# Optimization experiments

Hardware: AMD Instinct MI355X
Metric: run time of the kernel (lower is better)

## Reference

```python
import jax, jax.numpy as jnp
import numpy as np

N_RETRIEVAL = 10  # config['n_retrieval']


def setup_inputs() -> dict:
    key = jax.random.key(0)
    kq, kk, ko = jax.random.split(key, 3)
    Q, N, D = 256, 10000, 128
    C, H, W = 4, 84, 84
    q = jax.random.normal(kq, (Q, D), dtype=jnp.float32)
    k = jax.random.normal(kk, (N, D), dtype=jnp.float32)
    obs = jax.random.uniform(ko, (N, C, H, W), dtype=jnp.float32)
    return {"q": q, "k": k, "obs": obs}


def reference(q, k, obs):
    # Squared euclidean distances [Q, N] (same ordering as sklearn's
    # euclidean kneighbors; sqrt is monotone so top-k indices match).
    q2 = jnp.sum(q * q, axis=1, keepdims=True)            # [Q, 1]
    k2 = jnp.sum(k * k, axis=1)                            # [N]
    sqdist = q2 - 2.0 * (q @ k.T) + k2[None, :]            # [Q, N]
    # n_retrieval smallest distances -> indices [Q, K]
    _, indices = jax.lax.top_k(-sqdist, N_RETRIEVAL)
    # Gather observations: [Q, K, C, H, W]
    selected_obs = obs[indices]
    # permute(1, 0, 2, 3, 4) -> [K, Q, C, H, W]
    selected_obs = jnp.transpose(selected_obs, (1, 0, 2, 3, 4))
    return selected_obs
```

## Files before the change

### kernel.cpp

```cpp
#include <hip/hip_runtime.h>
#include <stdint.h>

#define QCNT 256
#define NKEYS 10000
#define DDIM 128
#define KSEL 10
#define OBSROW 28224

typedef float f4v __attribute__((ext_vector_type(4)));
typedef float f32x4 __attribute__((ext_vector_type(4)));
typedef _Float16 f16x8 __attribute__((ext_vector_type(8)));

#define QTILE 16
#define KCHUNK 48
#define NTILES 3
#define NCHUNK_M ((NKEYS + KCHUNK - 1) / KCHUNK)
#define LISTM 10

__device__ inline unsigned long long enc_key(float d, int n) {
  unsigned u = __float_as_uint(d);
  u ^= (unsigned)((int)u >> 31) | 0x80000000u;
  return ((unsigned long long)u << 32) | (unsigned)n;
}

__device__ inline unsigned long long wave_min_u64(unsigned long long w) {
#pragma unroll
  for (int off = 1; off < 64; off <<= 1) {
    unsigned long long o =
        (unsigned long long)__shfl_xor((long long)w, off, 64);
    if (o < w) w = o;
  }
  return w;
}

__device__ inline void insert10(unsigned long long best[LISTM],
                                unsigned long long key) {
  if (key < best[LISTM - 1]) {
    best[LISTM - 1] = key;
#pragma unroll
    for (int s = LISTM - 1; s >= 1; --s) {
      if (best[s] < best[s - 1]) {
        unsigned long long t = best[s];
        best[s] = best[s - 1];
        best[s - 1] = t;
      }
    }
  }
}

__global__ __launch_bounds__(64) void knn_part_fused(
    const float* __restrict__ q, const float* __restrict__ k,
    unsigned long long* __restrict__ part) {
  const int qt   = blockIdx.x;
  const int ch   = blockIdx.y;
  const int lane = threadIdx.x;
  const int lq   = lane & 15;
  const int lk8  = (lane >> 4) * 8;
  const int q0   = qt * QTILE;

  f16x8 bh[4], bl[4];
  {
    const float* qrow = q + (size_t)(q0 + lq) * DDIM + lk8;
#pragma unroll
    for (int kc = 0; kc < 4; ++kc) {
      f4v v0 = *(const f4v*)(qrow + kc * 32);
      f4v v1 = *(const f4v*)(qrow + kc * 32 + 4);
      float e[8] = {v0.x, v0.y, v0.z, v0.w, v1.x, v1.y, v1.z, v1.w};
#pragma unroll
      for (int j = 0; j < 8; ++j) {
        _Float16 h = (_Float16)e[j];
        bh[kc][j]  = h;
        bl[kc][j]  = (_Float16)(e[j] - (float)h);
      }
    }
  }

  unsigned long long list[LISTM];
#pragma unroll
  for (int s = 0; s < LISTM; ++s) list[s] = ~0ULL;

  const int kbase = ch * KCHUNK;
#pragma unroll
  for (int t = 0; t < NTILES; ++t) {
    const int tb  = kbase + t * 16;
    int row       = tb + lq;
    if (row > NKEYS - 1) row = NKEYS - 1;
    const float* arow = k + (size_t)row * DDIM + lk8;

    f32x4 acc = {0.f, 0.f, 0.f, 0.f};
    float k2p = 0.f;
#pragma unroll
    for (int kc = 0; kc < 4; ++kc) {
      f4v a0 = *(const f4v*)(arow + kc * 32);
      f4v a1 = *(const f4v*)(arow + kc * 32 + 4);
      float e[8] = {a0.x, a0.y, a0.z, a0.w, a1.x, a1.y, a1.z, a1.w};
      f16x8 ah, al;
#pragma unroll
      for (int j = 0; j < 8; ++j) {
        _Float16 h = (_Float16)e[j];
        ah[j]      = h;
        al[j]      = (_Float16)(e[j] - (float)h);
        k2p        = fmaf(e[j], e[j], k2p);
      }
      acc = __builtin_amdgcn_mfma_f32_16x16x32_f16(ah, bh[kc], acc, 0, 0, 0);
      acc = __builtin_amdgcn_mfma_f32_16x16x32_f16(ah, bl[kc], acc, 0, 0, 0);
      acc = __builtin_amdgcn_mfma_f32_16x16x32_f16(al, bh[kc], acc, 0, 0, 0);
    }

    k2p += __shfl_xor(k2p, 16, 64);
    k2p += __shfl_xor(k2p, 32, 64);
    const int rb = (lane >> 4) * 4;
    const int r0 = tb + rb;
#pragma unroll
    for (int reg = 0; reg < 4; ++reg) {
      float k2v = __shfl(k2p, rb + reg, 64);
      const int n = r0 + reg;
      if (n < NKEYS) {
        insert10(list, enc_key(fmaf(-2.f, acc[reg], k2v), n));
      }
    }
  }

  unsigned long long* dst =
      part + ((size_t)(q0 + lq) * NCHUNK_M + ch) * KSEL;
#pragma unroll 1
  for (int r = 0; r < KSEL; ++r) {
    unsigned long long w = list[0];
    {
      unsigned long long o =
          (unsigned long long)__shfl_xor((long long)w, 16, 64);
      if (o < w) w = o;
      o = (unsigned long long)__shfl_xor((long long)w, 32, 64);
      if (o < w) w = o;
    }
    if (list[0] == w) {
#pragma unroll
      for (int s = 0; s < LISTM - 1; ++s) list[s] = list[s + 1];
      list[LISTM - 1] = ~0ULL;
    }
    if (lane < 16) dst[r] = w;
  }
}

template <int NCHUNK_T>
__global__ __launch_bounds__(256) void knn_merge_gather_kernel(
    const float* __restrict__ obs, const unsigned long long* __restrict__ part,
    float* __restrict__ out) {
  constexpr int NCAND_T = NCHUNK_T * KSEL;
  constexpr int SLOTS   = (NCAND_T + 63) / 64;

  const int b    = blockIdx.x;
  const int r    = b >> 8;
  const int qq   = b & 255;
  const int tid  = threadIdx.x;

  __shared__ int s_src;

  if (tid < 64) {
    const unsigned long long* cp = part + (size_t)qq * NCAND_T;
    unsigned long long c[SLOTS];
#pragma unroll
    for (int i = 0; i < SLOTS; ++i) {
      const int idx = tid + 64 * i;
      c[i] = (idx < NCAND_T) ? cp[idx] : ~0ULL;
    }
    unsigned long long w = ~0ULL;
#pragma unroll 1
    for (int round = 0; round <= r; ++round) {
      unsigned long long m = c[0];
#pragma unroll
      for (int i = 1; i < SLOTS; ++i) m = (c[i] < m) ? c[i] : m;
      w = wave_min_u64(m);
#pragma unroll
      for (int i = 0; i < SLOTS; ++i)
        if (c[i] == w) c[i] = ~0ULL;
    }
    if (tid == 0) s_src = (int)(w & 0xffffffffu);
  }
  __syncthreads();
  const int src = __builtin_amdgcn_readfirstlane(s_src);

  const f4v* __restrict__ s = (const f4v*)(obs + (size_t)src * OBSROW);
  f4v* __restrict__ d       = (f4v*)(out + (size_t)b * OBSROW);
#pragma unroll 4
  for (int i = tid; i < OBSROW / 4; i += 256) {
    f4v v = s[i];
    __builtin_nontemporal_store(v, &d[i]);
  }
}

extern "C" void kernel_launch(void* const* d_in, const int* in_sizes, int n_in,
                              void* d_out, int out_size, void* d_ws,
                              size_t ws_size, hipStream_t stream) {
  const float* q   = (const float*)d_in[0];
  const float* k   = (const float*)d_in[1];
  const float* obs = (const float*)d_in[2];
  float* out = (float*)d_out;

  unsigned long long* part = (unsigned long long*)d_ws;

  knn_part_fused<<<dim3(QCNT / QTILE, NCHUNK_M), 64, 0, stream>>>(q, k, part);
  knn_merge_gather_kernel<NCHUNK_M>
      <<<KSEL * QCNT, 256, 0, stream>>>(obs, part, out);
}
```

Measured before the change: 117.3 us.

## Split merge from gather so each query's top-k merge runs once

The old fused kernel had every one of the 2560 gather blocks redo the candidate merge for its query, looping up to r+1 selection rounds over ~2090 candidates. The merge now runs once per query in its own kernel (one wave per query) and writes the 10 indices to workspace. A separate gather kernel reads the index and copies the observation row. This removes about tenfold redundant merge work and leaves the gather blocks free of a serial prefix, at the cost of an extra kernel launch and a small workspace round trip.

```diff
diff --git a/kernel.cpp b/kernel.cpp
--- a/kernel.cpp
+++ b/kernel.cpp
@@ -82,8 +82,8 @@
   const int kbase = ch * KCHUNK;
 #pragma unroll
   for (int t = 0; t < NTILES; ++t) {
-    const int tb  = kbase + t * 16;
-    int row       = tb + lq;
+    const int tb = kbase + t * 16;
+    int row      = tb + lq;
     if (row > NKEYS - 1) row = NKEYS - 1;
     const float* arow = k + (size_t)row * DDIM + lk8;
 
@@ -143,47 +143,47 @@
 }
 
 template <int NCHUNK_T>
-__global__ __launch_bounds__(256) void knn_merge_gather_kernel(
-    const float* __restrict__ obs, const unsigned long long* __restrict__ part,
-    float* __restrict__ out) {
+__global__ __launch_bounds__(256) void knn_merge_kernel(
+    const unsigned long long* __restrict__ part, int* __restrict__ out_idx) {
   constexpr int NCAND_T = NCHUNK_T * KSEL;
   constexpr int SLOTS   = (NCAND_T + 63) / 64;
 
-  const int b    = blockIdx.x;
-  const int r    = b >> 8;
-  const int qq   = b & 255;
-  const int tid  = threadIdx.x;
-
-  __shared__ int s_src;
-
-  if (tid < 64) {
-    const unsigned long long* cp = part + (size_t)qq * NCAND_T;
-    unsigned long long c[SLOTS];
-#pragma unroll
-    for (int i = 0; i < SLOTS; ++i) {
-      const int idx = tid + 64 * i;
-      c[i] = (idx < NCAND_T) ? cp[idx] : ~0ULL;
-    }
-    unsigned long long w = ~0ULL;
+  const int wv   = threadIdx.x >> 6;
+  const int lane = threadIdx.x & 63;
+  const int qq   = blockIdx.x * 4 + wv;
+
+  const unsigned long long* cp = part + (size_t)qq * NCAND_T;
+  unsigned long long c[SLOTS];
+#pragma unroll
+  for (int i = 0; i < SLOTS; ++i) {
+    const int idx = lane + 64 * i;
+    c[i] = (idx < NCAND_T) ? cp[idx] : ~0ULL;
+  }
 #pragma unroll 1
-    for (int round = 0; round <= r; ++round) {
-      unsigned long long m = c[0];
-#pragma unroll
-      for (int i = 1; i < SLOTS; ++i) m = (c[i] < m) ? c[i] : m;
-      w = wave_min_u64(m);
-#pragma unroll
-      for (int i = 0; i < SLOTS; ++i)
-        if (c[i] == w) c[i] = ~0ULL;
-    }
-    if (tid == 0) s_src = (int)(w & 0xffffffffu);
-  }
-  __syncthreads();
-  const int src = __builtin_amdgcn_readfirstlane(s_src);
+  for (int r = 0; r < KSEL; ++r) {
+    unsigned long long m = c[0];
+#pragma unroll
+    for (int i = 1; i < SLOTS; ++i) m = (c[i] < m) ? c[i] : m;
+    const unsigned long long w = wave_min_u64(m);
+#pragma unroll
+    for (int i = 0; i < SLOTS; ++i)
+      if (c[i] == w) c[i] = ~0ULL;
+    if (lane == 0) out_idx[qq * KSEL + r] = (int)(w & 0xffffffffu);
+  }
+}
+
+__global__ __launch_bounds__(256) void knn_gather_kernel(
+    const float* __restrict__ obs, const int* __restrict__ idx,
+    float* __restrict__ out) {
+  const int b  = blockIdx.x;
+  const int r  = b >> 8;
+  const int qq = b & 255;
+  const int src = __builtin_amdgcn_readfirstlane(idx[qq * KSEL + r]);
 
   const f4v* __restrict__ s = (const f4v*)(obs + (size_t)src * OBSROW);
   f4v* __restrict__ d       = (f4v*)(out + (size_t)b * OBSROW);
 #pragma unroll 4
-  for (int i = tid; i < OBSROW / 4; i += 256) {
+  for (int i = threadIdx.x; i < OBSROW / 4; i += 256) {
     f4v v = s[i];
     __builtin_nontemporal_store(v, &d[i]);
   }
@@ -198,8 +198,9 @@
   float* out = (float*)d_out;
 
   unsigned long long* part = (unsigned long long*)d_ws;
+  int* idx_ws = (int*)((char*)d_ws + (size_t)QCNT * NCHUNK_M * KSEL * 8);
 
   knn_part_fused<<<dim3(QCNT / QTILE, NCHUNK_M), 64, 0, stream>>>(q, k, part);
-  knn_merge_gather_kernel<NCHUNK_M>
-      <<<KSEL * QCNT, 256, 0, stream>>>(obs, part, out);
-}
+  knn_merge_kernel<NCHUNK_M><<<QCNT / 4, 256, 0, stream>>>(part, idx_ws);
+  knn_gather_kernel<<<KSEL * QCNT, 256, 0, stream>>>(obs, idx_ws, out);
+}
```

Result: slower. 123.5 us (+5.3%).
